# Optimization experiments

Measured on AMD Instinct MI355X. Metric: run time of the kernel, lower is better.

The kernel has to match this reference:

```python
import jax, jax.numpy as jnp
import numpy as np

N = 50000
E = 400000
H = 8          # heads
NEG_SLOPE = 0.2  # PyG GATConv default negative_slope
DIMS = [(128, 32), (32, 16), (16, 32)]  # (in, per-head out) for conv1..3


def setup_inputs() -> dict:
    key = jax.random.key(0)
    ks = jax.random.split(key, 2 + 4 * len(DIMS))
    inp = {
        "x": jax.random.normal(ks[0], (N, DIMS[0][0]), jnp.float32),
        "edge_index": jax.random.randint(ks[1], (2, E), 0, N, jnp.int32),
    }
    ki = 2
    for li, (din, dout) in enumerate(DIMS, 1):
        glorot = 1.0 / np.sqrt(din)
        inp[f"W{li}"] = jax.random.normal(ks[ki], (din, H * dout), jnp.float32) * glorot; ki += 1
        inp[f"as{li}"] = jax.random.normal(ks[ki], (H, dout), jnp.float32) * 0.1; ki += 1
        inp[f"ad{li}"] = jax.random.normal(ks[ki], (H, dout), jnp.float32) * 0.1; ki += 1
        inp[f"b{li}"] = jnp.zeros((dout,), jnp.float32); ki += 1
    return inp


def gat_conv(x, src, dst, W, att_s, att_d, b):
    """PyG GATConv with concat=False (mean over heads), self-loops already appended."""
    n = x.shape[0]
    h, c = att_s.shape
    xp = (x @ W).reshape(n, h, c)                     # [N,H,C] projected per-head feats
    a_s = jnp.einsum('nhc,hc->nh', xp, att_s)          # [N,H]
    a_d = jnp.einsum('nhc,hc->nh', xp, att_d)
    e = jax.nn.leaky_relu(a_s[src] + a_d[dst], NEG_SLOPE)   # [E',H]
    m = jax.ops.segment_max(e, dst, num_segments=n)          # stable softmax per dst node
    ex = jnp.exp(e - m[dst])
    s = jax.ops.segment_sum(ex, dst, num_segments=n)
    alpha = ex / s[dst]                                      # [E',H]
    out = jax.ops.segment_sum(xp[src] * alpha[:, :, None], dst, num_segments=n)  # [N,H,C]
    return out.mean(axis=1) + b


def reference(x, edge_index, W1, as1, ad1, b1, W2, as2, ad2, b2, W3, as3, ad3, b3):
    n = x.shape[0]
    loop = jnp.arange(n, dtype=edge_index.dtype)  # add self-loops (PyG default)
    src = jnp.concatenate([edge_index[0], loop])
    dst = jnp.concatenate([edge_index[1], loop])
    h1 = jax.nn.relu(gat_conv(x, src, dst, W1, as1, ad1, b1))
    h2 = jax.nn.relu(gat_conv(h1, src, dst, W2, as2, ad2, b2))
    h3 = jax.nn.relu(gat_conv(h2, src, dst, W3, as3, ad3, b3))
    return jnp.concatenate([h1, h2, h3], axis=1)  # [N, 32+16+32]
```

## Files before the change

kernel.cpp:

```cpp
#include <hip/hip_runtime.h>
#include <hip/hip_fp16.h>
#include <math.h>

#define NHEAD 8
#define NEG_SLOPE 0.2f
#define OUT_COLS 80

__device__ __forceinline__ float lrelu(float x) {
    return x > 0.f ? x : NEG_SLOPE * x;
}

template<int HC, int C>
__device__ __forceinline__ void proj_epilogue(
    const float (&acc)[32], int n, int n_nodes, int j0, int j0u,
    const float* __restrict__ as_flat, const float* __restrict__ ad_flat,
    __half* __restrict__ xp, float* __restrict__ a_s, float* __restrict__ a_d) {
    float ps[2] = {0.f, 0.f}, pd[2] = {0.f, 0.f};
#pragma unroll
    for (int q = 0; q < 32; ++q) {
        const int g = (C == 16 && q >= 16) ? 1 : 0;
        ps[g] += acc[q] * as_flat[j0u + q];
        pd[g] += acc[q] * ad_flat[j0u + q];
    }
    if (n < n_nodes) {
        __half2 buf[16];
#pragma unroll
        for (int q = 0; q < 16; ++q)
            buf[q] = __float22half2_rn(make_float2(acc[2 * q], acc[2 * q + 1]));
        float4* dst = (float4*)(xp + (size_t)n * HC + j0);
        const float4* srcb = (const float4*)buf;
#pragma unroll
        for (int q = 0; q < 4; ++q) dst[q] = srcb[q];
        if (C == 32) {
            const int h = j0 / 32;
            a_s[(size_t)n * NHEAD + h] = ps[0];
            a_d[(size_t)n * NHEAD + h] = pd[0];
        } else {
            const int h = j0 / 16;
            a_s[(size_t)n * NHEAD + h] = ps[0];
            a_s[(size_t)n * NHEAD + h + 1] = ps[1];
            a_d[(size_t)n * NHEAD + h] = pd[0];
            a_d[(size_t)n * NHEAD + h + 1] = pd[1];
        }
    }
}

template<int DIN, int HC, int C>
__global__ __launch_bounds__(256) void proj_kernel(
    const float* __restrict__ xin, int xstride, int xoff,
    const float* __restrict__ W,
    const float* __restrict__ as_flat, const float* __restrict__ ad_flat,
    __half* __restrict__ xp, float* __restrict__ a_s, float* __restrict__ a_d,
    int n_nodes) {
    const int lane = threadIdx.x & 63;
    const int wv = threadIdx.x >> 6;
    const int j0 = blockIdx.x * 128 + wv * 32;
    const int j0u = __builtin_amdgcn_readfirstlane(j0);
    const int n0 = blockIdx.y * 128 + lane;
    const int nlast = n_nodes - 1;
    const int nc0 = min(n0, nlast);
    const int nc1 = min(n0 + 64, nlast);

    float acc0[32], acc1[32];
#pragma unroll
    for (int q = 0; q < 32; ++q) { acc0[q] = 0.f; acc1[q] = 0.f; }

    const float* __restrict__ xr0 = xin + (size_t)nc0 * xstride + xoff;
    const float* __restrict__ xr1 = xin + (size_t)nc1 * xstride + xoff;

#pragma unroll 2
    for (int k4 = 0; k4 < DIN / 4; ++k4) {
        const float4 xv0 = *(const float4*)(xr0 + k4 * 4);
        const float4 xv1 = *(const float4*)(xr1 + k4 * 4);
#pragma unroll
        for (int kk = 0; kk < 4; ++kk) {
            const float xk0 = kk == 0 ? xv0.x : kk == 1 ? xv0.y : kk == 2 ? xv0.z : xv0.w;
            const float xk1 = kk == 0 ? xv1.x : kk == 1 ? xv1.y : kk == 2 ? xv1.z : xv1.w;
            const float4* __restrict__ W4 =
                (const float4*)(W + (size_t)(k4 * 4 + kk) * HC + j0u);
#pragma unroll
            for (int q = 0; q < 8; ++q) {
                const float4 wq = W4[q];
                acc0[q * 4 + 0] += xk0 * wq.x;  acc1[q * 4 + 0] += xk1 * wq.x;
                acc0[q * 4 + 1] += xk0 * wq.y;  acc1[q * 4 + 1] += xk1 * wq.y;
                acc0[q * 4 + 2] += xk0 * wq.z;  acc1[q * 4 + 2] += xk1 * wq.z;
                acc0[q * 4 + 3] += xk0 * wq.w;  acc1[q * 4 + 3] += xk1 * wq.w;
            }
        }
    }
    proj_epilogue<HC, C>(acc0, n0, n_nodes, j0, j0u, as_flat, ad_flat, xp, a_s, a_d);
    proj_epilogue<HC, C>(acc1, n0 + 64, n_nodes, j0, j0u, as_flat, ad_flat, xp, a_s, a_d);
}

__global__ void hist_kernel(const int* __restrict__ ei, int E, int* __restrict__ deg) {
    const int e = blockIdx.x * blockDim.x + threadIdx.x;
    if (e < E) atomicAdd(&deg[ei[E + e]], 1);
}

__global__ __launch_bounds__(256) void blocksum_kernel(const int* __restrict__ deg, int N,
                                                       int* __restrict__ bsum) {
    __shared__ int red[256];
    const int t = threadIdx.x;
    const int base = blockIdx.x * 1024 + t * 4;
    int s = 0;
    if (base + 3 < N) {
        const int4 v = *(const int4*)(deg + base);
        s = v.x + v.y + v.z + v.w;
    } else {
#pragma unroll
        for (int i = 0; i < 4; ++i) if (base + i < N) s += deg[base + i];
    }
    red[t] = s;
    __syncthreads();
    for (int off = 128; off > 0; off >>= 1) {
        if (t < off) red[t] += red[t + off];
        __syncthreads();
    }
    if (t == 0) bsum[blockIdx.x] = red[0];
}

__global__ __launch_bounds__(64) void bscan_kernel(int* __restrict__ bsum, int NB) {
    const int lane = threadIdx.x;
    int run = 0;
    for (int base = 0; base < NB; base += 64) {
        const int i = base + lane;
        const int v = (i < NB) ? bsum[i] : 0;
        int inc = v;
#pragma unroll
        for (int off = 1; off < 64; off <<= 1) {
            const int u = __shfl_up(inc, off, 64);
            if (lane >= off) inc += u;
        }
        if (i < NB) bsum[i] = run + inc - v;
        run += __shfl(inc, 63, 64);
    }
}

__global__ __launch_bounds__(256) void rowptr_kernel(const int* __restrict__ deg,
                                                     const int* __restrict__ bsum,
                                                     int N, int E,
                                                     int* __restrict__ rowptr,
                                                     int* __restrict__ cursor) {
    __shared__ int tsum[256];
    const int t = threadIdx.x;
    const int base = blockIdx.x * 1024 + t * 4;
    int v[4];
    int s = 0;
#pragma unroll
    for (int i = 0; i < 4; ++i) {
        v[i] = (base + i < N) ? deg[base + i] : 0;
        s += v[i];
    }
    tsum[t] = s;
    __syncthreads();
    for (int off = 1; off < 256; off <<= 1) {
        const int u = (t >= off) ? tsum[t - off] : 0;
        __syncthreads();
        tsum[t] += u;
        __syncthreads();
    }
    int run = bsum[blockIdx.x] + tsum[t] - s;
#pragma unroll
    for (int i = 0; i < 4; ++i) {
        if (base + i < N) {
            rowptr[base + i] = run;
            cursor[base + i] = run;
            run += v[i];
        }
    }
    if (blockIdx.x == 0 && t == 0) rowptr[N] = E;
}

__global__ void scatter_kernel(const int* __restrict__ ei, int E,
                               int* __restrict__ cursor, int* __restrict__ csr_src) {
    const int e = blockIdx.x * blockDim.x + threadIdx.x;
    if (e < E) {
        const int pos = atomicAdd(&cursor[ei[E + e]], 1);
        csr_src[pos] = ei[e];
    }
}

template<int C>
__global__ __launch_bounds__(256) void aggr_kernel(
    const int* __restrict__ rowptr, const int* __restrict__ csr_src,
    const float* __restrict__ a_s, const float* __restrict__ a_d,
    const __half* __restrict__ xp, const float* __restrict__ bias,
    float* __restrict__ out, int out_off, int N) {
    constexpr int HC = NHEAD * C;
    constexpr int LPE = HC / 8;
    constexpr int EPW = 64 / LPE;
    constexpr int CQ = C / 8;
    const int n = (blockIdx.x * blockDim.x + threadIdx.x) >> 6;
    if (n >= N) return;
    const int lane = threadIdx.x & 63;
    const int iA = lane >> 3, hA = lane & 7;
    const int le = lane & (LPE - 1);
    const int epar = lane / LPE;
    const int h = le / CQ;
    const int c0 = (le % CQ) * 8;
    const int row0 = rowptr[n];
    const int deg = rowptr[n + 1] - row0;
    const int items = deg + 1;

    const float adhA = a_d[(size_t)n * NHEAD + hA];
    float sacc = 0.f;
    float acc[8];
#pragma unroll
    for (int j = 0; j < 8; ++j) acc[j] = 0.f;

    for (int base = 0; base < items; base += 8) {
        const int idx = base + iA;
        int src = n;
        float ex = 0.f;
        if (idx < items) {
            if (idx < deg) src = csr_src[row0 + idx];
            ex = expf(lrelu(a_s[(size_t)src * NHEAD + hA] + adhA));
        }
        sacc += ex;
#pragma unroll
        for (int g = 0; g < 8; g += EPW) {
            const int it = g + epar;
            const int srcb = __shfl(src, it * 8, 64);
            const float exb = __shfl(ex, it * 8 + h, 64);
            const float4 r = *(const float4*)(xp + (size_t)srcb * HC + h * C + c0);
            const __half2* h2 = (const __half2*)&r;
#pragma unroll
            for (int q = 0; q < 4; ++q) {
                const float2 f = __half22float2(h2[q]);
                acc[2 * q]     += exb * f.x;
                acc[2 * q + 1] += exb * f.y;
            }
        }
    }
    sacc += __shfl_xor(sacc, 8, 64);
    sacc += __shfl_xor(sacc, 16, 64);
    sacc += __shfl_xor(sacc, 32, 64);
    const float sinv = 1.f / __shfl(sacc, h, 64);

#pragma unroll
    for (int off = LPE; off < 64; off <<= 1) {
#pragma unroll
        for (int j = 0; j < 8; ++j) acc[j] += __shfl_xor(acc[j], off, 64);
    }
#pragma unroll
    for (int j = 0; j < 8; ++j) acc[j] *= sinv;
#pragma unroll
    for (int off = CQ; off < LPE; off <<= 1) {
#pragma unroll
        for (int j = 0; j < 8; ++j) acc[j] += __shfl_xor(acc[j], off, 64);
    }
    if (lane < CQ) {
        float v[8];
#pragma unroll
        for (int j = 0; j < 8; ++j)
            v[j] = fmaxf(acc[j] * (1.f / NHEAD) + bias[lane * 8 + j], 0.f);
        float* op = out + (size_t)n * OUT_COLS + out_off + lane * 8;
        *(float4*)op = make_float4(v[0], v[1], v[2], v[3]);
        *(float4*)(op + 4) = make_float4(v[4], v[5], v[6], v[7]);
    }
}

static inline size_t align_up(size_t x) { return (x + 255) & ~size_t(255); }

extern "C" void kernel_launch(void* const* d_in, const int* in_sizes, int n_in,
                              void* d_out, int out_size, void* d_ws, size_t ws_size,
                              hipStream_t stream) {
    const float* x  = (const float*)d_in[0];
    const int*   ei = (const int*)d_in[1];
    const float* W1  = (const float*)d_in[2];
    const float* as1 = (const float*)d_in[3];
    const float* ad1 = (const float*)d_in[4];
    const float* b1  = (const float*)d_in[5];
    const float* W2  = (const float*)d_in[6];
    const float* as2 = (const float*)d_in[7];
    const float* ad2 = (const float*)d_in[8];
    const float* b2  = (const float*)d_in[9];
    const float* W3  = (const float*)d_in[10];
    const float* as3 = (const float*)d_in[11];
    const float* ad3 = (const float*)d_in[12];
    const float* b3  = (const float*)d_in[13];
    float* out = (float*)d_out;

    const int N = in_sizes[0] / 128;
    const int E = in_sizes[1] / 2;

    char* w = (char*)d_ws;
    __half* xp    = (__half*)w; w += align_up((size_t)N * 256 * 2);
    float* a_s    = (float*)w;  w += align_up((size_t)N * NHEAD * 4);
    float* a_d    = (float*)w;  w += align_up((size_t)N * NHEAD * 4);
    int*   deg    = (int*)w;    w += align_up((size_t)N * 4);
    int*   rowptr = (int*)w;    w += align_up((size_t)(N + 1) * 4);
    int*   cursor = (int*)w;    w += align_up((size_t)N * 4);
    int*   csrsrc = (int*)w;    w += align_up((size_t)E * 4);
    int*   bsum   = (int*)w;    w += align_up(((size_t)N / 1024 + 2) * 4);

    const int EB = 256;
    const int eg = (E + EB - 1) / EB;
    const int ntiles = (N + 127) / 128;
    const int ngrid = (N + 3) / 4;
    const int NB = (N + 1023) / 1024;

    hipMemsetAsync(deg, 0, (size_t)N * 4, stream);
    hist_kernel<<<eg, EB, 0, stream>>>(ei, E, deg);
    blocksum_kernel<<<NB, 256, 0, stream>>>(deg, N, bsum);
    bscan_kernel<<<1, 64, 0, stream>>>(bsum, NB);
    rowptr_kernel<<<NB, 256, 0, stream>>>(deg, bsum, N, E, rowptr, cursor);
    scatter_kernel<<<eg, EB, 0, stream>>>(ei, E, cursor, csrsrc);

    proj_kernel<128, 256, 32><<<dim3(2, ntiles), 256, 0, stream>>>(
        x, 128, 0, W1, as1, ad1, xp, a_s, a_d, N);
    aggr_kernel<32><<<ngrid, 256, 0, stream>>>(rowptr, csrsrc, a_s, a_d, xp, b1, out, 0, N);

    proj_kernel<32, 128, 16><<<dim3(1, ntiles), 256, 0, stream>>>(
        out, OUT_COLS, 0, W2, as2, ad2, xp, a_s, a_d, N);
    aggr_kernel<16><<<ngrid, 256, 0, stream>>>(rowptr, csrsrc, a_s, a_d, xp, b2, out, 32, N);

    proj_kernel<16, 256, 32><<<dim3(2, ntiles), 256, 0, stream>>>(
        out, OUT_COLS, 32, W3, as3, ad3, xp, a_s, a_d, N);
    aggr_kernel<32><<<ngrid, 256, 0, stream>>>(rowptr, csrsrc, a_s, a_d, xp, b3, out, 48, N);
}
```

Measured before the change: 260.4 us.

## Use fp16 MFMA for per-layer projections with pre-swizzled weight fragments

Replaces the scalar FP32 FMA projection kernel with one built on the mfma_f32_16x16x32_f16 matrix instruction. Each wave computes a 16-node tile across all output columns. A new prep kernel converts and re-lays out W1..W3 into fp16 fragment order once per call. Results are staged through LDS so the epilogue can store fp16 rows and compute the a_s/a_d dot products with shuffle reductions. This cuts ALU cost of the projection, but inputs and weights are now rounded to fp16 before the multiply, and an extra small kernel launch is added.

```diff
diff --git a/kernel.cpp b/kernel.cpp
--- a/kernel.cpp
+++ b/kernel.cpp
@@ -6,90 +6,142 @@
 #define NEG_SLOPE 0.2f
 #define OUT_COLS 80
 
+typedef _Float16 f16x8 __attribute__((ext_vector_type(8)));
+typedef float f32x4 __attribute__((ext_vector_type(4)));
+
 __device__ __forceinline__ float lrelu(float x) {
     return x > 0.f ? x : NEG_SLOPE * x;
 }
 
-template<int HC, int C>
-__device__ __forceinline__ void proj_epilogue(
-    const float (&acc)[32], int n, int n_nodes, int j0, int j0u,
-    const float* __restrict__ as_flat, const float* __restrict__ ad_flat,
-    __half* __restrict__ xp, float* __restrict__ a_s, float* __restrict__ a_d) {
-    float ps[2] = {0.f, 0.f}, pd[2] = {0.f, 0.f};
-#pragma unroll
-    for (int q = 0; q < 32; ++q) {
-        const int g = (C == 16 && q >= 16) ? 1 : 0;
-        ps[g] += acc[q] * as_flat[j0u + q];
-        pd[g] += acc[q] * ad_flat[j0u + q];
-    }
-    if (n < n_nodes) {
-        __half2 buf[16];
-#pragma unroll
-        for (int q = 0; q < 16; ++q)
-            buf[q] = __float22half2_rn(make_float2(acc[2 * q], acc[2 * q + 1]));
-        float4* dst = (float4*)(xp + (size_t)n * HC + j0);
-        const float4* srcb = (const float4*)buf;
-#pragma unroll
-        for (int q = 0; q < 4; ++q) dst[q] = srcb[q];
-        if (C == 32) {
-            const int h = j0 / 32;
-            a_s[(size_t)n * NHEAD + h] = ps[0];
-            a_d[(size_t)n * NHEAD + h] = pd[0];
-        } else {
-            const int h = j0 / 16;
-            a_s[(size_t)n * NHEAD + h] = ps[0];
-            a_s[(size_t)n * NHEAD + h + 1] = ps[1];
-            a_d[(size_t)n * NHEAD + h] = pd[0];
-            a_d[(size_t)n * NHEAD + h + 1] = pd[1];
-        }
+__device__ __forceinline__ void prep32_frag(const float* __restrict__ W,
+                                            __half* __restrict__ Wf,
+                                            int HC, int NT, int t, int DINLIM) {
+    const int lane = t & 63, f = t >> 6;
+    const int kc = f / NT, nt = f % NT;
+    const int col = nt * 16 + (lane & 15);
+    const int kb = kc * 32 + ((lane >> 4) << 2);
+    __half v[8];
+#pragma unroll
+    for (int j = 0; j < 8; ++j) {
+        const int k = kb + (j & 3) + ((j >> 2) << 4);
+        v[j] = (k < DINLIM) ? __float2half(W[k * HC + col]) : __half(0.f);
+    }
+    *(float4*)(Wf + (size_t)t * 8) = *(float4*)&v[0];
+}
+
+__global__ __launch_bounds__(256) void prep_all(
+    const float* __restrict__ W1, const float* __restrict__ W2,
+    const float* __restrict__ W3,
+    __half* __restrict__ Wf1, __half* __restrict__ Wf2, __half* __restrict__ Wf3) {
+    const int b = blockIdx.x, tid = threadIdx.x;
+    if (b < 16) {
+        prep32_frag(W1, Wf1, 256, 16, b * 256 + tid, 128);
+    } else if (b < 18) {
+        const int t = (b - 16) * 256 + tid;
+        if (t < 512) prep32_frag(W2, Wf2, 128, 8, t, 32);
+    } else {
+        const int t = (b - 18) * 256 + tid;
+        if (t < 1024) prep32_frag(W3, Wf3, 256, 16, t, 16);
     }
 }
 
 template<int DIN, int HC, int C>
-__global__ __launch_bounds__(256) void proj_kernel(
+__global__ __launch_bounds__(256) void proj_mfma(
     const float* __restrict__ xin, int xstride, int xoff,
-    const float* __restrict__ W,
+    const __half* __restrict__ Wf,
     const float* __restrict__ as_flat, const float* __restrict__ ad_flat,
     __half* __restrict__ xp, float* __restrict__ a_s, float* __restrict__ a_d,
     int n_nodes) {
+    constexpr int NT = HC / 16;
+    __shared__ __half lds[4][16][HC + 8];
     const int lane = threadIdx.x & 63;
     const int wv = threadIdx.x >> 6;
-    const int j0 = blockIdx.x * 128 + wv * 32;
-    const int j0u = __builtin_amdgcn_readfirstlane(j0);
-    const int n0 = blockIdx.y * 128 + lane;
+    const int n0 = (blockIdx.x * 4 + wv) * 16;
     const int nlast = n_nodes - 1;
-    const int nc0 = min(n0, nlast);
-    const int nc1 = min(n0 + 64, nlast);
-
-    float acc0[32], acc1[32];
-#pragma unroll
-    for (int q = 0; q < 32; ++q) { acc0[q] = 0.f; acc1[q] = 0.f; }
-
-    const float* __restrict__ xr0 = xin + (size_t)nc0 * xstride + xoff;
-    const float* __restrict__ xr1 = xin + (size_t)nc1 * xstride + xoff;
-
-#pragma unroll 2
-    for (int k4 = 0; k4 < DIN / 4; ++k4) {
-        const float4 xv0 = *(const float4*)(xr0 + k4 * 4);
-        const float4 xv1 = *(const float4*)(xr1 + k4 * 4);
-#pragma unroll
-        for (int kk = 0; kk < 4; ++kk) {
-            const float xk0 = kk == 0 ? xv0.x : kk == 1 ? xv0.y : kk == 2 ? xv0.z : xv0.w;
-            const float xk1 = kk == 0 ? xv1.x : kk == 1 ? xv1.y : kk == 2 ? xv1.z : xv1.w;
-            const float4* __restrict__ W4 =
-                (const float4*)(W + (size_t)(k4 * 4 + kk) * HC + j0u);
-#pragma unroll
-            for (int q = 0; q < 8; ++q) {
-                const float4 wq = W4[q];
-                acc0[q * 4 + 0] += xk0 * wq.x;  acc1[q * 4 + 0] += xk1 * wq.x;
-                acc0[q * 4 + 1] += xk0 * wq.y;  acc1[q * 4 + 1] += xk1 * wq.y;
-                acc0[q * 4 + 2] += xk0 * wq.z;  acc1[q * 4 + 2] += xk1 * wq.z;
-                acc0[q * 4 + 3] += xk0 * wq.w;  acc1[q * 4 + 3] += xk1 * wq.w;
+    const int ar = min(n0 + (lane & 15), nlast);
+    const int kb = (lane >> 4) << 2;
+    const float* __restrict__ xr = xin + (size_t)ar * xstride + xoff;
+
+    f32x4 acc[NT];
+#pragma unroll
+    for (int nt = 0; nt < NT; ++nt) acc[nt] = (f32x4){0.f, 0.f, 0.f, 0.f};
+
+    if constexpr (DIN >= 32) {
+        constexpr int KCNT = DIN / 32;
+#pragma unroll
+        for (int kc = 0; kc < KCNT; ++kc) {
+            const float4 xv0 = *(const float4*)(xr + kc * 32 + kb);
+            const float4 xv1 = *(const float4*)(xr + kc * 32 + 16 + kb);
+            f16x8 af;
+            af[0] = (_Float16)xv0.x; af[1] = (_Float16)xv0.y;
+            af[2] = (_Float16)xv0.z; af[3] = (_Float16)xv0.w;
+            af[4] = (_Float16)xv1.x; af[5] = (_Float16)xv1.y;
+            af[6] = (_Float16)xv1.z; af[7] = (_Float16)xv1.w;
+            const __half* __restrict__ Wb = Wf + ((size_t)kc * NT * 64 + lane) * 8;
+#pragma unroll
+            for (int nt = 0; nt < NT; ++nt) {
+                const f16x8 bf = *(const f16x8*)(Wb + (size_t)nt * 64 * 8);
+                acc[nt] = __builtin_amdgcn_mfma_f32_16x16x32_f16(af, bf, acc[nt], 0, 0, 0);
             }
         }
-    }
-    proj_epilogue<HC, C>(acc0, n0, n_nodes, j0, j0u, as_flat, ad_flat, xp, a_s, a_d);
-    proj_epilogue<HC, C>(acc1, n0 + 64, n_nodes, j0, j0u, as_flat, ad_flat, xp, a_s, a_d);
+    } else {
+        const float4 xv0 = *(const float4*)(xr + kb);
+        f16x8 af;
+        af[0] = (_Float16)xv0.x; af[1] = (_Float16)xv0.y;
+        af[2] = (_Float16)xv0.z; af[3] = (_Float16)xv0.w;
+        af[4] = (_Float16)0.f; af[5] = (_Float16)0.f;
+        af[6] = (_Float16)0.f; af[7] = (_Float16)0.f;
+        const __half* __restrict__ Wb = Wf + (size_t)lane * 8;
+#pragma unroll
+        for (int nt = 0; nt < NT; ++nt) {
+            const f16x8 bf = *(const f16x8*)(Wb + (size_t)nt * 64 * 8);
+            acc[nt] = __builtin_amdgcn_mfma_f32_16x16x32_f16(af, bf, acc[nt], 0, 0, 0);
+        }
+    }
+
+#pragma unroll
+    for (int nt = 0; nt < NT; ++nt) {
+#pragma unroll
+        for (int r = 0; r < 4; ++r)
+            lds[wv][kb + r][nt * 16 + (lane & 15)] = __float2half(acc[nt][r]);
+    }
+
+    constexpr int F4PR = HC / 8;
+    constexpr int ITER = 16 * F4PR / 64;
+    constexpr int LPH = C / 8;
+#pragma unroll
+    for (int i = 0; i < ITER; ++i) {
+        const int flat = i * 64 + lane;
+        const int row = flat / F4PR;
+        const int co = (flat % F4PR) * 8;
+        const int node = n0 + row;
+        __half hv[8];
+        *(float4*)hv = *(const float4*)&lds[wv][row][co];
+        const float4 as0 = *(const float4*)(as_flat + co);
+        const float4 as1 = *(const float4*)(as_flat + co + 4);
+        const float4 ad0 = *(const float4*)(ad_flat + co);
+        const float4 ad1 = *(const float4*)(ad_flat + co + 4);
+        float xv[8];
+#pragma unroll
+        for (int j = 0; j < 8; ++j) xv[j] = __half2float(hv[j]);
+        float ps = xv[0] * as0.x + xv[1] * as0.y + xv[2] * as0.z + xv[3] * as0.w
+                 + xv[4] * as1.x + xv[5] * as1.y + xv[6] * as1.z + xv[7] * as1.w;
+        float pd = xv[0] * ad0.x + xv[1] * ad0.y + xv[2] * ad0.z + xv[3] * ad0.w
+                 + xv[4] * ad1.x + xv[5] * ad1.y + xv[6] * ad1.z + xv[7] * ad1.w;
+#pragma unroll
+        for (int off = 1; off < LPH; off <<= 1) {
+            ps += __shfl_xor(ps, off, 64);
+            pd += __shfl_xor(pd, off, 64);
+        }
+        if (node <= nlast) {
+            *(float4*)(xp + (size_t)node * HC + co) = *(float4*)hv;
+            if ((flat & (LPH - 1)) == 0) {
+                const int h = co / C;
+                a_s[(size_t)node * NHEAD + h] = ps;
+                a_d[(size_t)node * NHEAD + h] = pd;
+            }
+        }
+    }
 }
 
 __global__ void hist_kernel(const int* __restrict__ ei, int E, int* __restrict__ deg) {
@@ -293,29 +345,33 @@
     int*   cursor = (int*)w;    w += align_up((size_t)N * 4);
     int*   csrsrc = (int*)w;    w += align_up((size_t)E * 4);
     int*   bsum   = (int*)w;    w += align_up(((size_t)N / 1024 + 2) * 4);
+    __half* Wf1   = (__half*)w; w += align_up((size_t)128 * 256 * 2);
+    __half* Wf2   = (__half*)w; w += align_up((size_t)32 * 128 * 2);
+    __half* Wf3   = (__half*)w; w += align_up((size_t)32 * 256 * 2);
 
     const int EB = 256;
     const int eg = (E + EB - 1) / EB;
-    const int ntiles = (N + 127) / 128;
+    const int pgrid = (N + 63) / 64;
     const int ngrid = (N + 3) / 4;
     const int NB = (N + 1023) / 1024;
 
-    hipMemsetAsync(deg, 0, (size_t)N * 4, stream);
+    prep_all<<<22, 256, 0, stream>>>(W1, W2, W3, Wf1, Wf2, Wf3);
+    (void)hipMemsetAsync(deg, 0, (size_t)N * 4, stream);
     hist_kernel<<<eg, EB, 0, stream>>>(ei, E, deg);
     blocksum_kernel<<<NB, 256, 0, stream>>>(deg, N, bsum);
     bscan_kernel<<<1, 64, 0, stream>>>(bsum, NB);
     rowptr_kernel<<<NB, 256, 0, stream>>>(deg, bsum, N, E, rowptr, cursor);
     scatter_kernel<<<eg, EB, 0, stream>>>(ei, E, cursor, csrsrc);
 
-    proj_kernel<128, 256, 32><<<dim3(2, ntiles), 256, 0, stream>>>(
-        x, 128, 0, W1, as1, ad1, xp, a_s, a_d, N);
+    proj_mfma<128, 256, 32><<<pgrid, 256, 0, stream>>>(
+        x, 128, 0, Wf1, as1, ad1, xp, a_s, a_d, N);
     aggr_kernel<32><<<ngrid, 256, 0, stream>>>(rowptr, csrsrc, a_s, a_d, xp, b1, out, 0, N);
 
-    proj_kernel<32, 128, 16><<<dim3(1, ntiles), 256, 0, stream>>>(
-        out, OUT_COLS, 0, W2, as2, ad2, xp, a_s, a_d, N);
+    proj_mfma<32, 128, 16><<<pgrid, 256, 0, stream>>>(
+        out, OUT_COLS, 0, Wf2, as2, ad2, xp, a_s, a_d, N);
     aggr_kernel<16><<<ngrid, 256, 0, stream>>>(rowptr, csrsrc, a_s, a_d, xp, b2, out, 32, N);
 
-    proj_kernel<16, 256, 32><<<dim3(2, ntiles), 256, 0, stream>>>(
-        out, OUT_COLS, 32, W3, as3, ad3, xp, a_s, a_d, N);
+    proj_mfma<16, 256, 32><<<pgrid, 256, 0, stream>>>(
+        out, OUT_COLS, 32, Wf3, as3, ad3, xp, a_s, a_d, N);
     aggr_kernel<32><<<ngrid, 256, 0, stream>>>(rowptr, csrsrc, a_s, a_d, xp, b3, out, 48, N);
 }
```

Result: faster. 220.3 us (-15.4%).
